# Kernel optimization log

Measured on AMD Instinct MI355X. Metric: run time of the kernel, lower is better.

The kernel has to match this reference:

```python
import jax, jax.numpy as jnp
import numpy as np
from jax import lax

WINDOW = 11
SIGMA = 1.5
K1 = 0.01
K2 = 0.03
DATA_RANGE = 1.0


def _gaussian_kernel(channels):
    coords = jnp.arange(WINDOW, dtype=jnp.float32) - (WINDOW // 2)
    g = jnp.exp(-(coords ** 2) / (2.0 * SIGMA ** 2))
    g = g / g.sum()
    k2d = g[:, None] * g[None, :]                      # [W, W]
    # depthwise kernel, OIHW with I=1, O=channels (feature_group_count=channels)
    return jnp.broadcast_to(k2d, (channels, 1, WINDOW, WINDOW))


def _depthwise_blur(img, kernel, channels):
    pad = WINDOW // 2
    return lax.conv_general_dilated(
        img, kernel,
        window_strides=(1, 1),
        padding=[(pad, pad), (pad, pad)],
        dimension_numbers=('NCHW', 'OIHW', 'NCHW'),
        feature_group_count=channels,
    )


def setup_inputs() -> dict:
    key = jax.random.key(0)
    kx, ky = jax.random.split(key)
    shape = (16, 3, 512, 512)
    x = jax.random.uniform(kx, shape, dtype=jnp.float32)
    y = jax.random.uniform(ky, shape, dtype=jnp.float32)
    return {"x": x, "y": y}


def reference(x, y):
    channels = x.shape[1]
    kernel = _gaussian_kernel(channels)

    mu_x = _depthwise_blur(x, kernel, channels)
    mu_y = _depthwise_blur(y, kernel, channels)
    mu_x_sq = mu_x * mu_x
    mu_y_sq = mu_y * mu_y
    mu_xy = mu_x * mu_y

    sigma_x_sq = _depthwise_blur(x * x, kernel, channels) - mu_x_sq
    sigma_y_sq = _depthwise_blur(y * y, kernel, channels) - mu_y_sq
    sigma_xy = _depthwise_blur(x * y, kernel, channels) - mu_xy

    C1 = (K1 * DATA_RANGE) ** 2
    C2 = (K2 * DATA_RANGE) ** 2
    numerator = (2.0 * mu_xy + C1) * (2.0 * sigma_xy + C2)
    denominator = (mu_x_sq + mu_y_sq + C1) * (sigma_x_sq + sigma_y_sq + C2)
    ssim_map = numerator / (denominator + 1e-8)
    return 1.0 - ssim_map.mean()
```

## Files before the change

### kernel.cpp

```cpp
#include <hip/hip_runtime.h>
#include <cmath>

#define WIN 11
#define HALO 5
#define IMG 512
#define TW 64
#define TH 16
#define RH (TH + 2*HALO)
#define SH2 72
#define NIMG 48
#define NPIX (16.0 * 3.0 * 512.0 * 512.0)
#define CPR (IMG/2)
#define NPART (NIMG * (IMG/4))

typedef _Float16 f16;
typedef _Float16 h2 __attribute__((ext_vector_type(2)));

struct GaussW { float w[WIN]; };

__device__ __forceinline__ unsigned pk2(float a, float b) {
    auto h = __builtin_amdgcn_cvt_pkrtz(a, b);
    return __builtin_bit_cast(unsigned, h);
}
__device__ __forceinline__ h2 uph(unsigned u) {
    return __builtin_bit_cast(h2, u);
}

__global__ void __launch_bounds__(64) zero_kernel(float* out) {
    if (threadIdx.x == 0) out[0] = 0.f;
}

__global__ void __launch_bounds__(64) finish_kernel(float* out) {
    if (threadIdx.x == 0)
        out[0] = 1.0f - out[0] * (float)(1.0 / NPIX);
}

__global__ void __launch_bounds__(256) k1_hblur(
        const float* __restrict__ xin, const float* __restrict__ yin,
        uint4* __restrict__ ws, int imgOff, GaussW W) {
    const int tid = threadIdx.x;
    const int c   = tid & 127;
    const int row = blockIdx.y * 2 + (tid >> 7);
    const int lz  = blockIdx.z;
    const size_t rbase = ((size_t)(imgOff + lz) * IMG + row) * IMG;
    const float* xr = xin + rbase;
    const float* yr = yin + rbase;
    const int gx0 = c * 4 - 5;

    float xv[14], yv[14];
    if (c >= 2 && c <= 125) {
        xv[0] = xr[gx0];  yv[0] = yr[gx0];
        #pragma unroll
        for (int q = 0; q < 3; ++q) {
            float4 a = *(const float4*)(xr + gx0 + 1 + 4*q);
            float4 b = *(const float4*)(yr + gx0 + 1 + 4*q);
            xv[1+4*q] = a.x; xv[2+4*q] = a.y; xv[3+4*q] = a.z; xv[4+4*q] = a.w;
            yv[1+4*q] = b.x; yv[2+4*q] = b.y; yv[3+4*q] = b.z; yv[4+4*q] = b.w;
        }
        xv[13] = xr[gx0 + 13];  yv[13] = yr[gx0 + 13];
    } else {
        #pragma unroll
        for (int j = 0; j < 14; ++j) {
            int gx = gx0 + j;
            bool ok = ((unsigned)gx < IMG);
            xv[j] = ok ? xr[gx] : 0.f;
            yv[j] = ok ? yr[gx] : 0.f;
        }
    }

    float ax[4]  = {0,0,0,0}, ay[4] = {0,0,0,0};
    float as[4]  = {0,0,0,0}, axy[4] = {0,0,0,0};
    #pragma unroll
    for (int j = 0; j < 14; ++j) {
        float xs = xv[j], ys = yv[j];
        float xy = xs * ys;
        float ss = fmaf(xs, xs, ys * ys);
        #pragma unroll
        for (int o = 0; o < 4; ++o) {
            int k = j - o;
            if (k >= 0 && k < WIN) {
                float wk = W.w[k];
                ax[o]  += wk * xs;
                ay[o]  += wk * ys;
                as[o]  += wk * ss;
                axy[o] += wk * xy;
            }
        }
    }

    const size_t ob = ((size_t)lz * IMG + row) * CPR + 2 * c;
    uint4 u0, u1;
    u0.x = pk2(ax[0],  ax[1]);  u0.y = pk2(ay[0],  ay[1]);
    u0.z = pk2(as[0],  as[1]);  u0.w = pk2(axy[0], axy[1]);
    u1.x = pk2(ax[2],  ax[3]);  u1.y = pk2(ay[2],  ay[3]);
    u1.z = pk2(as[2],  as[3]);  u1.w = pk2(axy[2], axy[3]);
    ws[ob]     = u0;
    ws[ob + 1] = u1;
}

__global__ void __launch_bounds__(256) k2_vblur(
        const uint4* __restrict__ ws, float* __restrict__ partial,
        int imgOff, GaussW W) {
    const int cp = threadIdx.x;
    const int lz = blockIdx.x;
    const int by = blockIdx.y;
    const int r0 = by * 4 - HALO;
    const size_t base = (size_t)lz * IMG * CPR + cp;
    __shared__ float wsum[4];

    h2 w2[WIN];
    #pragma unroll
    for (int k = 0; k < WIN; ++k) {
        f16 wk = (f16)W.w[k];
        w2[k] = (h2){wk, wk};
    }

    uint4 v[14];
    if (by >= 2 && by <= 125) {
        #pragma unroll
        for (int j = 0; j < 14; ++j)
            v[j] = ws[base + (size_t)(r0 + j) * CPR];
    } else {
        #pragma unroll
        for (int j = 0; j < 14; ++j) {
            int r = r0 + j;
            v[j] = ((unsigned)r < IMG) ? ws[base + (size_t)r * CPR]
                                       : make_uint4(0u, 0u, 0u, 0u);
        }
    }

    const float C1 = 0.01f * 0.01f;
    const float C2 = 0.03f * 0.03f;
    float local = 0.f;
    #pragma unroll
    for (int o = 0; o < 4; ++o) {
        h2 a0 = (h2){(f16)0,(f16)0}, a1 = a0, a2 = a0, a3 = a0;
        #pragma unroll
        for (int k = 0; k < WIN; ++k) {
            uint4 u = v[o + k];
            h2 wk = w2[k];
            a0 += wk * uph(u.x);
            a1 += wk * uph(u.y);
            a2 += wk * uph(u.z);
            a3 += wk * uph(u.w);
        }
        #pragma unroll
        for (int h = 0; h < 2; ++h) {
            float mux = (float)a0[h];
            float muy = (float)a1[h];
            float es  = (float)a2[h];
            float exy = (float)a3[h];
            float mux2 = mux * mux, muy2 = muy * muy, muxy = mux * muy;
            float num = (2.f * muxy + C1) * (2.f * (exy - muxy) + C2);
            float den = (mux2 + muy2 + C1) * ((es - mux2 - muy2) + C2);
            local += num * __builtin_amdgcn_rcpf(den + 1e-8f);
        }
    }

    #pragma unroll
    for (int off = 32; off > 0; off >>= 1)
        local += __shfl_down(local, off, 64);
    if ((cp & 63) == 0) wsum[cp >> 6] = local;
    __syncthreads();
    if (cp == 0)
        partial[(size_t)(imgOff + lz) * (IMG/4) + by] =
            wsum[0] + wsum[1] + wsum[2] + wsum[3];
}

__global__ void __launch_bounds__(256) reduce_kernel(
        const float* __restrict__ partial, float* __restrict__ out) {
    __shared__ float wsum[4];
    const int tid = threadIdx.x;
    float s = 0.f;
    for (int i = tid; i < NPART; i += 256) s += partial[i];
    #pragma unroll
    for (int off = 32; off > 0; off >>= 1)
        s += __shfl_down(s, off, 64);
    if ((tid & 63) == 0) wsum[tid >> 6] = s;
    __syncthreads();
    if (tid == 0)
        out[0] = 1.0f - (wsum[0] + wsum[1] + wsum[2] + wsum[3]) * (float)(1.0 / NPIX);
}

__global__ void __launch_bounds__(256) fb_tile_kernel(
        const float* __restrict__ xin, const float* __restrict__ yin,
        float* __restrict__ out_acc, GaussW W) {
    __shared__ __align__(16) f16 hb[5][RH * SH2];
    __shared__ float wsum[4];
    const int tid = threadIdx.x;
    const int bx = blockIdx.x, by = blockIdx.y;
    const size_t ibase = (size_t)blockIdx.z * (IMG * IMG);
    const float* __restrict__ xb = xin + ibase;
    const float* __restrict__ yb = yin + ibase;

    if (tid < RH * (TW / 8)) {
        const int r  = tid >> 3;
        const int cg = tid & 7;
        const int gy  = by * TH - HALO + r;
        const int gx0 = bx * TW - HALO + cg * 8;
        float xv[18], yv[18];
        const float* xr = xb + (size_t)gy * IMG;
        const float* yr = yb + (size_t)gy * IMG;
        const bool interior = (bx >= 1 && bx <= 6 && by >= 1 && by <= 30);
        if (interior) {
            xv[0] = xr[gx0];  yv[0] = yr[gx0];
            #pragma unroll
            for (int q = 0; q < 4; ++q) {
                float4 a = *(const float4*)(xr + gx0 + 1 + 4*q);
                float4 b = *(const float4*)(yr + gx0 + 1 + 4*q);
                xv[1+4*q] = a.x; xv[2+4*q] = a.y; xv[3+4*q] = a.z; xv[4+4*q] = a.w;
                yv[1+4*q] = b.x; yv[2+4*q] = b.y; yv[3+4*q] = b.z; yv[4+4*q] = b.w;
            }
            xv[17] = xr[gx0 + 17];  yv[17] = yr[gx0 + 17];
        } else {
            const bool rowok = ((unsigned)gy < IMG);
            #pragma unroll
            for (int j = 0; j < 18; ++j) {
                int gx = gx0 + j;
                bool ok = rowok && ((unsigned)gx < IMG);
                xv[j] = ok ? xr[gx] : 0.f;
                yv[j] = ok ? yr[gx] : 0.f;
            }
        }
        float ax[8]={0,0,0,0,0,0,0,0}, ay[8]={0,0,0,0,0,0,0,0};
        float axx[8]={0,0,0,0,0,0,0,0}, ayy[8]={0,0,0,0,0,0,0,0}, axy[8]={0,0,0,0,0,0,0,0};
        #pragma unroll
        for (int j = 0; j < 18; ++j) {
            float xs = xv[j], ys = yv[j];
            float xx = xs*xs, yy = ys*ys, xy = xs*ys;
            #pragma unroll
            for (int o = 0; o < 8; ++o) {
                int k = j - o;
                if (k >= 0 && k < WIN) {
                    float wk = W.w[k];
                    ax[o]+=wk*xs; ay[o]+=wk*ys; axx[o]+=wk*xx; ayy[o]+=wk*yy; axy[o]+=wk*xy;
                }
            }
        }
        const int ob = r * SH2 + cg * 8;
        uint4 u;
        u.x=pk2(ax[0],ax[1]); u.y=pk2(ax[2],ax[3]); u.z=pk2(ax[4],ax[5]); u.w=pk2(ax[6],ax[7]);
        *(uint4*)&hb[0][ob] = u;
        u.x=pk2(ay[0],ay[1]); u.y=pk2(ay[2],ay[3]); u.z=pk2(ay[4],ay[5]); u.w=pk2(ay[6],ay[7]);
        *(uint4*)&hb[1][ob] = u;
        u.x=pk2(axx[0],axx[1]); u.y=pk2(axx[2],axx[3]); u.z=pk2(axx[4],axx[5]); u.w=pk2(axx[6],axx[7]);
        *(uint4*)&hb[2][ob] = u;
        u.x=pk2(ayy[0],ayy[1]); u.y=pk2(ayy[2],ayy[3]); u.z=pk2(ayy[4],ayy[5]); u.w=pk2(ayy[6],ayy[7]);
        *(uint4*)&hb[3][ob] = u;
        u.x=pk2(axy[0],axy[1]); u.y=pk2(axy[2],axy[3]); u.z=pk2(axy[4],axy[5]); u.w=pk2(axy[6],axy[7]);
        *(uint4*)&hb[4][ob] = u;
    }
    __syncthreads();

    const int c2 = tid & 31;
    const int r0 = (tid >> 5) << 1;
    const int hbase = 2 * c2;
    h2 w2[WIN];
    #pragma unroll
    for (int k = 0; k < WIN; ++k) { f16 wk = (f16)W.w[k]; w2[k] = (h2){wk, wk}; }
    h2 acc[5][2];
    #pragma unroll
    for (int f = 0; f < 5; ++f) { acc[f][0]=(h2){(f16)0,(f16)0}; acc[f][1]=(h2){(f16)0,(f16)0}; }
    #pragma unroll
    for (int f = 0; f < 5; ++f) {
        const f16* buf = hb[f];
        h2 v[12];
        #pragma unroll
        for (int k = 0; k < 12; ++k) v[k] = *(const h2*)&buf[(r0 + k) * SH2 + hbase];
        #pragma unroll
        for (int k = 0; k < WIN; ++k) { acc[f][0] += w2[k]*v[k]; acc[f][1] += w2[k]*v[k+1]; }
    }
    const float C1 = 0.01f * 0.01f;
    const float C2 = 0.03f * 0.03f;
    float local = 0.f;
    #pragma unroll
    for (int o = 0; o < 2; ++o)
        #pragma unroll
        for (int h = 0; h < 2; ++h) {
            float mux=(float)acc[0][o][h], muy=(float)acc[1][o][h];
            float exx=(float)acc[2][o][h], eyy=(float)acc[3][o][h], exy=(float)acc[4][o][h];
            float mux2=mux*mux, muy2=muy*muy, muxy=mux*muy;
            float num=(2.f*muxy+C1)*(2.f*(exy-muxy)+C2);
            float den=(mux2+muy2+C1)*((exx-mux2)+(eyy-muy2)+C2);
            local += num * __builtin_amdgcn_rcpf(den + 1e-8f);
        }
    #pragma unroll
    for (int off = 32; off > 0; off >>= 1) local += __shfl_down(local, off, 64);
    if ((tid & 63) == 0) wsum[tid >> 6] = local;
    __syncthreads();
    if (tid == 0) atomicAdd(out_acc, wsum[0]+wsum[1]+wsum[2]+wsum[3]);
}

extern "C" void kernel_launch(void* const* d_in, const int* in_sizes, int n_in,
                              void* d_out, int out_size, void* d_ws, size_t ws_size,
                              hipStream_t stream) {
    const float* x = (const float*)d_in[0];
    const float* y = (const float*)d_in[1];
    float* out = (float*)d_out;

    GaussW gw;
    double g[WIN], s = 0.0;
    for (int i = 0; i < WIN; ++i) {
        double d = (double)(i - WIN / 2);
        g[i] = exp(-(d * d) / (2.0 * 1.5 * 1.5));
        s += g[i];
    }
    for (int i = 0; i < WIN; ++i) gw.w[i] = (float)(g[i] / s);

    auto need = [](int n) { return (size_t)n * IMG * CPR * sizeof(uint4); };
    int chunk = NIMG;
    while (chunk > 3 && need(chunk) + NPART * 4 > ws_size) chunk >>= 1;

    if (need(chunk) + NPART * 4 <= ws_size) {
        uint4* ws      = (uint4*)d_ws;
        float* partial = (float*)((char*)d_ws + need(chunk));
        for (int off = 0; off < NIMG; off += chunk) {
            hipLaunchKernelGGL(k1_hblur, dim3(1, IMG/2, chunk), dim3(256), 0, stream,
                               x, y, ws, off, gw);
            hipLaunchKernelGGL(k2_vblur, dim3(chunk, IMG/4, 1), dim3(256), 0, stream,
                               ws, partial, off, gw);
        }
        hipLaunchKernelGGL(reduce_kernel, dim3(1), dim3(256), 0, stream, partial, out);
    } else {
        hipLaunchKernelGGL(zero_kernel, dim3(1), dim3(64), 0, stream, out);
        hipLaunchKernelGGL(fb_tile_kernel, dim3(IMG/TW, IMG/TH, NIMG), dim3(256),
                           0, stream, x, y, out, gw);
        hipLaunchKernelGGL(finish_kernel, dim3(1), dim3(64), 0, stream, out);
    }
}
```

Before: 168.5 us.

## Fuse horizontal and vertical blur into one tiled kernel using shared memory

Replaces the two-pass design, which wrote horizontally blurred fp16 moments to global workspace and read them back, with one fused kernel. Each block computes a 64x64 output tile, keeps the horizontal blur of a 74-row halo region in LDS, and then runs the vertical blur and SSIM reduction from LDS. This removes the global write and read of the intermediate buffer. In exchange it recomputes halo rows (74/64 overhead) and uses about 38 KB of LDS per block, which may limit occupancy.

```diff
diff --git a/kernel.cpp b/kernel.cpp
--- a/kernel.cpp
+++ b/kernel.cpp
@@ -4,14 +4,12 @@
 #define WIN 11
 #define HALO 5
 #define IMG 512
-#define TW 64
-#define TH 16
-#define RH (TH + 2*HALO)
-#define SH2 72
 #define NIMG 48
+#define TS 64
+#define HR (TS + 2*HALO)
+#define NTILE (IMG/TS)
+#define NBLK (NIMG*NTILE*NTILE)
 #define NPIX (16.0 * 3.0 * 512.0 * 512.0)
-#define CPR (IMG/2)
-#define NPART (NIMG * (IMG/4))
 
 typedef _Float16 f16;
 typedef _Float16 h2 __attribute__((ext_vector_type(2)));
@@ -35,78 +33,86 @@
         out[0] = 1.0f - out[0] * (float)(1.0 / NPIX);
 }
 
-__global__ void __launch_bounds__(256) k1_hblur(
+template<int USE_ATOMIC>
+__global__ void __launch_bounds__(256) fused_ssim(
         const float* __restrict__ xin, const float* __restrict__ yin,
-        uint4* __restrict__ ws, int imgOff, GaussW W) {
+        float* __restrict__ outp, GaussW W) {
+    __shared__ uint4 hb[HR][32];
+    __shared__ float wsum[4];
     const int tid = threadIdx.x;
-    const int c   = tid & 127;
-    const int row = blockIdx.y * 2 + (tid >> 7);
-    const int lz  = blockIdx.z;
-    const size_t rbase = ((size_t)(imgOff + lz) * IMG + row) * IMG;
-    const float* xr = xin + rbase;
-    const float* yr = yin + rbase;
-    const int gx0 = c * 4 - 5;
-
-    float xv[14], yv[14];
-    if (c >= 2 && c <= 125) {
-        xv[0] = xr[gx0];  yv[0] = yr[gx0];
-        #pragma unroll
-        for (int q = 0; q < 3; ++q) {
-            float4 a = *(const float4*)(xr + gx0 + 1 + 4*q);
-            float4 b = *(const float4*)(yr + gx0 + 1 + 4*q);
-            xv[1+4*q] = a.x; xv[2+4*q] = a.y; xv[3+4*q] = a.z; xv[4+4*q] = a.w;
-            yv[1+4*q] = b.x; yv[2+4*q] = b.y; yv[3+4*q] = b.z; yv[4+4*q] = b.w;
-        }
-        xv[13] = xr[gx0 + 13];  yv[13] = yr[gx0 + 13];
-    } else {
-        #pragma unroll
-        for (int j = 0; j < 14; ++j) {
-            int gx = gx0 + j;
-            bool ok = ((unsigned)gx < IMG);
-            xv[j] = ok ? xr[gx] : 0.f;
-            yv[j] = ok ? yr[gx] : 0.f;
-        }
-    }
-
-    float ax[4]  = {0,0,0,0}, ay[4] = {0,0,0,0};
-    float as[4]  = {0,0,0,0}, axy[4] = {0,0,0,0};
-    #pragma unroll
-    for (int j = 0; j < 14; ++j) {
-        float xs = xv[j], ys = yv[j];
-        float xy = xs * ys;
-        float ss = fmaf(xs, xs, ys * ys);
-        #pragma unroll
-        for (int o = 0; o < 4; ++o) {
-            int k = j - o;
-            if (k >= 0 && k < WIN) {
-                float wk = W.w[k];
-                ax[o]  += wk * xs;
-                ay[o]  += wk * ys;
-                as[o]  += wk * ss;
-                axy[o] += wk * xy;
+    const int tx = blockIdx.x, ty = blockIdx.y;
+    const size_t ibase = (size_t)blockIdx.z * (size_t)(IMG * IMG);
+    const float* __restrict__ xb = xin + ibase;
+    const float* __restrict__ yb = yin + ibase;
+
+    const int cg  = tid & 15;
+    const int rr  = tid >> 4;
+    const int gx0 = tx * TS + cg * 4 - HALO;
+    const bool cint = (gx0 >= 0) && (gx0 + 13 < IMG);
+
+    #pragma unroll
+    for (int it = 0; it < 5; ++it) {
+        const int r = it * 16 + rr;
+        if (r < HR) {
+            const int gy = ty * TS - HALO + r;
+            if ((unsigned)gy < IMG) {
+                const float* xr = xb + (size_t)gy * IMG;
+                const float* yr = yb + (size_t)gy * IMG;
+                float xv[14], yv[14];
+                if (cint) {
+                    xv[0] = xr[gx0];  yv[0] = yr[gx0];
+                    #pragma unroll
+                    for (int q = 0; q < 3; ++q) {
+                        float4 a = *(const float4*)(xr + gx0 + 1 + 4*q);
+                        float4 b = *(const float4*)(yr + gx0 + 1 + 4*q);
+                        xv[1+4*q]=a.x; xv[2+4*q]=a.y; xv[3+4*q]=a.z; xv[4+4*q]=a.w;
+                        yv[1+4*q]=b.x; yv[2+4*q]=b.y; yv[3+4*q]=b.z; yv[4+4*q]=b.w;
+                    }
+                    xv[13] = xr[gx0 + 13];  yv[13] = yr[gx0 + 13];
+                } else {
+                    #pragma unroll
+                    for (int j = 0; j < 14; ++j) {
+                        int gx = gx0 + j;
+                        bool ok = ((unsigned)gx < IMG);
+                        xv[j] = ok ? xr[gx] : 0.f;
+                        yv[j] = ok ? yr[gx] : 0.f;
+                    }
+                }
+                float ax[4]  = {0,0,0,0}, ay[4]  = {0,0,0,0};
+                float as_[4] = {0,0,0,0}, axy[4] = {0,0,0,0};
+                #pragma unroll
+                for (int j = 0; j < 14; ++j) {
+                    float xs = xv[j], ys = yv[j];
+                    float xy = xs * ys;
+                    float ss = fmaf(xs, xs, ys * ys);
+                    #pragma unroll
+                    for (int o = 0; o < 4; ++o) {
+                        int k = j - o;
+                        if (k >= 0 && k < WIN) {
+                            float wk = W.w[k];
+                            ax[o]  += wk * xs;  ay[o]  += wk * ys;
+                            as_[o] += wk * ss;  axy[o] += wk * xy;
+                        }
+                    }
+                }
+                uint4 u0, u1;
+                u0.x = pk2(ax[0],  ax[1]);  u0.y = pk2(ay[0],  ay[1]);
+                u0.z = pk2(as_[0], as_[1]); u0.w = pk2(axy[0], axy[1]);
+                u1.x = pk2(ax[2],  ax[3]);  u1.y = pk2(ay[2],  ay[3]);
+                u1.z = pk2(as_[2], as_[3]); u1.w = pk2(axy[2], axy[3]);
+                hb[r][cg]      = u0;
+                hb[r][cg + 16] = u1;
+            } else {
+                uint4 z = make_uint4(0u, 0u, 0u, 0u);
+                hb[r][cg]      = z;
+                hb[r][cg + 16] = z;
             }
         }
     }
-
-    const size_t ob = ((size_t)lz * IMG + row) * CPR + 2 * c;
-    uint4 u0, u1;
-    u0.x = pk2(ax[0],  ax[1]);  u0.y = pk2(ay[0],  ay[1]);
-    u0.z = pk2(as[0],  as[1]);  u0.w = pk2(axy[0], axy[1]);
-    u1.x = pk2(ax[2],  ax[3]);  u1.y = pk2(ay[2],  ay[3]);
-    u1.z = pk2(as[2],  as[3]);  u1.w = pk2(axy[2], axy[3]);
-    ws[ob]     = u0;
-    ws[ob + 1] = u1;
-}
-
-__global__ void __launch_bounds__(256) k2_vblur(
-        const uint4* __restrict__ ws, float* __restrict__ partial,
-        int imgOff, GaussW W) {
-    const int cp = threadIdx.x;
-    const int lz = blockIdx.x;
-    const int by = blockIdx.y;
-    const int r0 = by * 4 - HALO;
-    const size_t base = (size_t)lz * IMG * CPR + cp;
-    __shared__ float wsum[4];
+    __syncthreads();
+
+    const int idx = tid & 31;
+    const int r0  = (tid >> 5) * 8;
 
     h2 w2[WIN];
     #pragma unroll
@@ -115,56 +121,55 @@
         w2[k] = (h2){wk, wk};
     }
 
-    uint4 v[14];
-    if (by >= 2 && by <= 125) {
-        #pragma unroll
-        for (int j = 0; j < 14; ++j)
-            v[j] = ws[base + (size_t)(r0 + j) * CPR];
-    } else {
-        #pragma unroll
-        for (int j = 0; j < 14; ++j) {
-            int r = r0 + j;
-            v[j] = ((unsigned)r < IMG) ? ws[base + (size_t)r * CPR]
-                                       : make_uint4(0u, 0u, 0u, 0u);
-        }
-    }
-
     const float C1 = 0.01f * 0.01f;
     const float C2 = 0.03f * 0.03f;
     float local = 0.f;
     #pragma unroll
-    for (int o = 0; o < 4; ++o) {
-        h2 a0 = (h2){(f16)0,(f16)0}, a1 = a0, a2 = a0, a3 = a0;
+    for (int half = 0; half < 2; ++half) {
+        const int rbase = r0 + half * 4;
+        uint4 v[14];
         #pragma unroll
-        for (int k = 0; k < WIN; ++k) {
-            uint4 u = v[o + k];
-            h2 wk = w2[k];
-            a0 += wk * uph(u.x);
-            a1 += wk * uph(u.y);
-            a2 += wk * uph(u.z);
-            a3 += wk * uph(u.w);
-        }
+        for (int j = 0; j < 14; ++j) v[j] = hb[rbase + j][idx];
         #pragma unroll
-        for (int h = 0; h < 2; ++h) {
-            float mux = (float)a0[h];
-            float muy = (float)a1[h];
-            float es  = (float)a2[h];
-            float exy = (float)a3[h];
-            float mux2 = mux * mux, muy2 = muy * muy, muxy = mux * muy;
-            float num = (2.f * muxy + C1) * (2.f * (exy - muxy) + C2);
-            float den = (mux2 + muy2 + C1) * ((es - mux2 - muy2) + C2);
-            local += num * __builtin_amdgcn_rcpf(den + 1e-8f);
+        for (int o = 0; o < 4; ++o) {
+            h2 a0 = (h2){(f16)0,(f16)0}, a1 = a0, a2 = a0, a3 = a0;
+            #pragma unroll
+            for (int k = 0; k < WIN; ++k) {
+                uint4 u = v[o + k];
+                h2 wk = w2[k];
+                a0 += wk * uph(u.x);
+                a1 += wk * uph(u.y);
+                a2 += wk * uph(u.z);
+                a3 += wk * uph(u.w);
+            }
+            #pragma unroll
+            for (int h = 0; h < 2; ++h) {
+                float mux = (float)a0[h];
+                float muy = (float)a1[h];
+                float es  = (float)a2[h];
+                float exy = (float)a3[h];
+                float mux2 = mux * mux, muy2 = muy * muy, muxy = mux * muy;
+                float num = (2.f * muxy + C1) * (2.f * (exy - muxy) + C2);
+                float den = (mux2 + muy2 + C1) * ((es - mux2 - muy2) + C2);
+                local += num * __builtin_amdgcn_rcpf(den + 1e-8f);
+            }
         }
     }
 
     #pragma unroll
     for (int off = 32; off > 0; off >>= 1)
         local += __shfl_down(local, off, 64);
-    if ((cp & 63) == 0) wsum[cp >> 6] = local;
+    if ((tid & 63) == 0) wsum[tid >> 6] = local;
     __syncthreads();
-    if (cp == 0)
-        partial[(size_t)(imgOff + lz) * (IMG/4) + by] =
-            wsum[0] + wsum[1] + wsum[2] + wsum[3];
+    if (tid == 0) {
+        float bs = wsum[0] + wsum[1] + wsum[2] + wsum[3];
+        if (USE_ATOMIC) {
+            atomicAdd(outp, bs);
+        } else {
+            int bid = (blockIdx.z * NTILE + blockIdx.y) * NTILE + blockIdx.x;
+            outp[bid] = bs;
+        }
+    }
 }
 
 __global__ void __launch_bounds__(256) reduce_kernel(
@@ -172,7 +177,7 @@
     __shared__ float wsum[4];
     const int tid = threadIdx.x;
     float s = 0.f;
-    for (int i = tid; i < NPART; i += 256) s += partial[i];
+    for (int i = tid; i < NBLK; i += 256) s += partial[i];
     #pragma unroll
     for (int off = 32; off > 0; off >>= 1)
         s += __shfl_down(s, off, 64);
@@ -182,115 +187,6 @@
         out[0] = 1.0f - (wsum[0] + wsum[1] + wsum[2] + wsum[3]) * (float)(1.0 / NPIX);
 }
 
-__global__ void __launch_bounds__(256) fb_tile_kernel(
-        const float* __restrict__ xin, const float* __restrict__ yin,
-        float* __restrict__ out_acc, GaussW W) {
-    __shared__ __align__(16) f16 hb[5][RH * SH2];
-    __shared__ float wsum[4];
-    const int tid = threadIdx.x;
-    const int bx = blockIdx.x, by = blockIdx.y;
-    const size_t ibase = (size_t)blockIdx.z * (IMG * IMG);
-    const float* __restrict__ xb = xin + ibase;
-    const float* __restrict__ yb = yin + ibase;
-
-    if (tid < RH * (TW / 8)) {
-        const int r  = tid >> 3;
-        const int cg = tid & 7;
-        const int gy  = by * TH - HALO + r;
-        const int gx0 = bx * TW - HALO + cg * 8;
-        float xv[18], yv[18];
-        const float* xr = xb + (size_t)gy * IMG;
-        const float* yr = yb + (size_t)gy * IMG;
-        const bool interior = (bx >= 1 && bx <= 6 && by >= 1 && by <= 30);
-        if (interior) {
-            xv[0] = xr[gx0];  yv[0] = yr[gx0];
-            #pragma unroll
-            for (int q = 0; q < 4; ++q) {
-                float4 a = *(const float4*)(xr + gx0 + 1 + 4*q);
-                float4 b = *(const float4*)(yr + gx0 + 1 + 4*q);
-                xv[1+4*q] = a.x; xv[2+4*q] = a.y; xv[3+4*q] = a.z; xv[4+4*q] = a.w;
-                yv[1+4*q] = b.x; yv[2+4*q] = b.y; yv[3+4*q] = b.z; yv[4+4*q] = b.w;
-            }
-            xv[17] = xr[gx0 + 17];  yv[17] = yr[gx0 + 17];
-        } else {
-            const bool rowok = ((unsigned)gy < IMG);
-            #pragma unroll
-            for (int j = 0; j < 18; ++j) {
-                int gx = gx0 + j;
-                bool ok = rowok && ((unsigned)gx < IMG);
-                xv[j] = ok ? xr[gx] : 0.f;
-                yv[j] = ok ? yr[gx] : 0.f;
-            }
-        }
-        float ax[8]={0,0,0,0,0,0,0,0}, ay[8]={0,0,0,0,0,0,0,0};
-        float axx[8]={0,0,0,0,0,0,0,0}, ayy[8]={0,0,0,0,0,0,0,0}, axy[8]={0,0,0,0,0,0,0,0};
-        #pragma unroll
-        for (int j = 0; j < 18; ++j) {
-            float xs = xv[j], ys = yv[j];
-            float xx = xs*xs, yy = ys*ys, xy = xs*ys;
-            #pragma unroll
-            for (int o = 0; o < 8; ++o) {
-                int k = j - o;
-                if (k >= 0 && k < WIN) {
-                    float wk = W.w[k];
-                    ax[o]+=wk*xs; ay[o]+=wk*ys; axx[o]+=wk*xx; ayy[o]+=wk*yy; axy[o]+=wk*xy;
-                }
-            }
-        }
-        const int ob = r * SH2 + cg * 8;
-        uint4 u;
-        u.x=pk2(ax[0],ax[1]); u.y=pk2(ax[2],ax[3]); u.z=pk2(ax[4],ax[5]); u.w=pk2(ax[6],ax[7]);
-        *(uint4*)&hb[0][ob] = u;
-        u.x=pk2(ay[0],ay[1]); u.y=pk2(ay[2],ay[3]); u.z=pk2(ay[4],ay[5]); u.w=pk2(ay[6],ay[7]);
-        *(uint4*)&hb[1][ob] = u;
-        u.x=pk2(axx[0],axx[1]); u.y=pk2(axx[2],axx[3]); u.z=pk2(axx[4],axx[5]); u.w=pk2(axx[6],axx[7]);
-        *(uint4*)&hb[2][ob] = u;
-        u.x=pk2(ayy[0],ayy[1]); u.y=pk2(ayy[2],ayy[3]); u.z=pk2(ayy[4],ayy[5]); u.w=pk2(ayy[6],ayy[7]);
-        *(uint4*)&hb[3][ob] = u;
-        u.x=pk2(axy[0],axy[1]); u.y=pk2(axy[2],axy[3]); u.z=pk2(axy[4],axy[5]); u.w=pk2(axy[6],axy[7]);
-        *(uint4*)&hb[4][ob] = u;
-    }
-    __syncthreads();
-
-    const int c2 = tid & 31;
-    const int r0 = (tid >> 5) << 1;
-    const int hbase = 2 * c2;
-    h2 w2[WIN];
-    #pragma unroll
-    for (int k = 0; k < WIN; ++k) { f16 wk = (f16)W.w[k]; w2[k] = (h2){wk, wk}; }
-    h2 acc[5][2];
-    #pragma unroll
-    for (int f = 0; f < 5; ++f) { acc[f][0]=(h2){(f16)0,(f16)0}; acc[f][1]=(h2){(f16)0,(f16)0}; }
-    #pragma unroll
-    for (int f = 0; f < 5; ++f) {
-        const f16* buf = hb[f];
-        h2 v[12];
-        #pragma unroll
-        for (int k = 0; k < 12; ++k) v[k] = *(const h2*)&buf[(r0 + k) * SH2 + hbase];
-        #pragma unroll
-        for (int k = 0; k < WIN; ++k) { acc[f][0] += w2[k]*v[k]; acc[f][1] += w2[k]*v[k+1]; }
-    }
-    const float C1 = 0.01f * 0.01f;
-    const float C2 = 0.03f * 0.03f;
-    float local = 0.f;
-    #pragma unroll
-    for (int o = 0; o < 2; ++o)
-        #pragma unroll
-        for (int h = 0; h < 2; ++h) {
-            float mux=(float)acc[0][o][h], muy=(float)acc[1][o][h];
-            float exx=(float)acc[2][o][h], eyy=(float)acc[3][o][h], exy=(float)acc[4][o][h];
-            float mux2=mux*mux, muy2=muy*muy, muxy=mux*muy;
-            float num=(2.f*muxy+C1)*(2.f*(exy-muxy)+C2);
-            float den=(mux2+muy2+C1)*((exx-mux2)+(eyy-muy2)+C2);
-            local += num * __builtin_amdgcn_rcpf(den + 1e-8f);
-        }
-    #pragma unroll
-    for (int off = 32; off > 0; off >>= 1) local += __shfl_down(local, off, 64);
-    if ((tid & 63) == 0) wsum[tid >> 6] = local;
-    __syncthreads();
-    if (tid == 0) atomicAdd(out_acc, wsum[0]+wsum[1]+wsum[2]+wsum[3]);
-}
-
 extern "C" void kernel_launch(void* const* d_in, const int* in_sizes, int n_in,
                               void* d_out, int out_size, void* d_ws, size_t ws_size,
                               hipStream_t stream) {
@@ -307,23 +203,15 @@
     }
     for (int i = 0; i < WIN; ++i) gw.w[i] = (float)(g[i] / s);
 
-    auto need = [](int n) { return (size_t)n * IMG * CPR * sizeof(uint4); };
-    int chunk = NIMG;
-    while (chunk > 3 && need(chunk) + NPART * 4 > ws_size) chunk >>= 1;
-
-    if (need(chunk) + NPART * 4 <= ws_size) {
-        uint4* ws      = (uint4*)d_ws;
-        float* partial = (float*)((char*)d_ws + need(chunk));
-        for (int off = 0; off < NIMG; off += chunk) {
-            hipLaunchKernelGGL(k1_hblur, dim3(1, IMG/2, chunk), dim3(256), 0, stream,
-                               x, y, ws, off, gw);
-            hipLaunchKernelGGL(k2_vblur, dim3(chunk, IMG/4, 1), dim3(256), 0, stream,
-                               ws, partial, off, gw);
-        }
-        hipLaunchKernelGGL(reduce_kernel, dim3(1), dim3(256), 0, stream, partial, out);
+    if (ws_size >= (size_t)NBLK * sizeof(float)) {
+        float* partial = (float*)d_ws;
+        hipLaunchKernelGGL((fused_ssim<0>), dim3(NTILE, NTILE, NIMG), dim3(256),
+                           0, stream, x, y, partial, gw);
+        hipLaunchKernelGGL(reduce_kernel, dim3(1), dim3(256), 0, stream,
+                           partial, out);
     } else {
         hipLaunchKernelGGL(zero_kernel, dim3(1), dim3(64), 0, stream, out);
-        hipLaunchKernelGGL(fb_tile_kernel, dim3(IMG/TW, IMG/TH, NIMG), dim3(256),
+        hipLaunchKernelGGL((fused_ssim<1>), dim3(NTILE, NTILE, NIMG), dim3(256),
                            0, stream, x, y, out, gw);
         hipLaunchKernelGGL(finish_kernel, dim3(1), dim3(64), 0, stream, out);
     }
```

Result: slower. 174.0 us (+3.2%).
